# Optimization experiments

Measured on AMD Instinct MI355X. Metric: run time of the kernel, lower is better.

The kernel has to match this reference:

```python
import jax, jax.numpy as jnp
import numpy as np

SCORE = 89; PERF = 300; R = SCORE + PERF   # roll_dims = score_1hot + perf_1hot
H = 1024; Z = 256; B = 64; T = 256
DUR, DY, IOI = 0, 100, 200                 # perf segment boundaries (durratio/dy/ioi)
BN_EPS = 1e-5

PARAM_SHAPES = [
    ("w_ih_f", (3*H, R)), ("w_hh_f", (3*H, H)), ("b_ih_f", (3*H,)), ("b_hh_f", (3*H,)),
    ("w_ih_b", (3*H, R)), ("w_hh_b", (3*H, H)), ("b_ih_b", (3*H,)), ("b_hh_b", (3*H,)),
    ("w_mu", (Z, 2*H)), ("b_mu", (Z,)), ("w_var", (Z, 2*H)), ("b_var", (Z,)),
    ("w_init", (H, Z)), ("b_init", (H,)),
    ("w_ih0", (3*H, Z + R)), ("w_hh0", (3*H, H)), ("b_ih0", (3*H,)), ("b_hh0", (3*H,)),
    ("w_ih1", (3*H, H)), ("w_hh1", (3*H, H)), ("b_ih1", (3*H,)), ("b_hh1", (3*H,)),
    ("w_ih2", (3*H, H)), ("w_hh2", (3*H, H)), ("b_ih2", (3*H,)), ("b_hh2", (3*H,)),
    ("w_out", (PERF, H)), ("b_out", (PERF,)),
]


def gru_cell(x, h, w_ih, w_hh, b_ih, b_hh):
    # torch GRU/GRUCell gate order: r, z, n
    gi = x @ w_ih.T + b_ih
    gh = h @ w_hh.T + b_hh
    i_r, i_z, i_n = jnp.split(gi, 3, axis=-1)
    h_r, h_z, h_n = jnp.split(gh, 3, axis=-1)
    r = jax.nn.sigmoid(i_r + h_r)
    zg = jax.nn.sigmoid(i_z + h_z)
    n = jnp.tanh(i_n + r * h_n)
    return (1.0 - zg) * n + zg * h


def setup_inputs() -> dict:
    key = jax.random.key(0)
    ks = jax.random.split(key, len(PARAM_SHAPES) + 1)
    inp = {"x": jax.random.normal(ks[0], (T, B, R), dtype=jnp.float32),
           "x_lengths": T}
    for i, (nm, shp) in enumerate(PARAM_SHAPES):
        inp[nm] = jax.random.normal(ks[i + 1], shp, dtype=jnp.float32) * 0.05
    return inp


def _forward(x, w_ih_f, w_hh_f, b_ih_f, b_hh_f, w_ih_b, w_hh_b, b_ih_b, b_hh_b,
             w_mu, b_mu, w_var, b_var, w_init, b_init,
             w_ih0, w_hh0, b_ih0, b_hh0, w_ih1, w_hh1, b_ih1, b_hh1,
             w_ih2, w_hh2, b_ih2, b_hh2, w_out, b_out):
    # ---- encode: bidirectional GRU, all lengths == T (pack == plain GRU) ----
    h0 = jnp.zeros((B, H), x.dtype)
    def run(xs, w_ih, w_hh, b_ih, b_hh):
        step = lambda h, xt: ((gru_cell(xt, h, w_ih, w_hh, b_ih, b_hh),) * 2)
        hT, _ = jax.lax.scan(step, h0, xs)
        return hT
    h_f = run(x, w_ih_f, w_hh_f, b_ih_f, b_hh_f)
    h_b = run(x[::-1], w_ih_b, w_hh_b, b_ih_b, b_hh_b)
    hidden = jnp.concatenate([h_f, h_b], axis=-1)          # [B, 2H]
    hidden = hidden / jnp.sqrt(1.0 + BN_EPS)               # BatchNorm2d(1) eval, fresh running stats
    mean = hidden @ w_mu.T + b_mu
    stddev = jnp.exp((hidden @ w_var.T + b_var) * 0.5)     # computed as in torch (unused in eval)
    z = mean                                               # eval-mode reparameterize -> mean
    score = x[:, :, :SCORE]                                # [T, B, SCORE]
    out0 = jnp.zeros((B, PERF), x.dtype).at[:, -1].set(1.0)
    sc0 = jnp.zeros((B, SCORE), x.dtype).at[:, -1].set(1.0)
    hinit = jnp.tanh(z @ w_init.T + b_init)                # hx[0] init
    def step(carry, xj):
        out, sc, hx0, hx1, hx2 = carry
        j, score_j = xj
        inp = jnp.concatenate([out, sc, z], axis=1)        # [B, PERF+SCORE+Z]
        hx0 = gru_cell(inp, hx0, w_ih0, w_hh0, b_ih0, b_hh0)
        hx1 = gru_cell(hx0, jnp.where(j == 0, hx0, hx1), w_ih1, w_hh1, b_ih1, b_hh1)
        hx2 = gru_cell(hx1, jnp.where(j == 0, hx1, hx2), w_ih2, w_hh2, b_ih2, b_hh2)
        logits = hx2 @ w_out.T + b_out                     # [B, PERF]
        o = jnp.concatenate([jax.nn.log_softmax(logits[:, DUR:DY], axis=1),
                             jax.nn.log_softmax(logits[:, DY:IOI], axis=1),
                             jax.nn.log_softmax(logits[:, IOI:], axis=1)], axis=1)
        out_next = jax.nn.one_hot(jnp.argmax(o, axis=1), PERF, dtype=o.dtype)  # eval sampling
        return (out_next, score_j, hx0, hx1, hx2), o
    _, outs = jax.lax.scan(step, (out0, sc0, hinit, hinit, hinit),
                           (jnp.arange(T), score))
    return outs.transpose(1, 0, 2)                         # [B, T, PERF]


def reference(x, x_lengths, w_ih_f, w_hh_f, b_ih_f, b_hh_f, w_ih_b, w_hh_b, b_ih_b, b_hh_b,
              w_mu, b_mu, w_var, b_var, w_init, b_init,
              w_ih0, w_hh0, b_ih0, b_hh0, w_ih1, w_hh1, b_ih1, b_hh1,
              w_ih2, w_hh2, b_ih2, b_hh2, w_out, b_out):
    outs = _forward(x, w_ih_f, w_hh_f, b_ih_f, b_hh_f, w_ih_b, w_hh_b, b_ih_b, b_hh_b,
                    w_mu, b_mu, w_var, b_var, w_init, b_init,
                    w_ih0, w_hh0, b_ih0, b_hh0, w_ih1, w_hh1, b_ih1, b_hh1,
                    w_ih2, w_hh2, b_ih2, b_hh2, w_out, b_out)
    zeros = jnp.zeros((B, Z), x.dtype)  # dis_mean / dis_stddev stay zero in eval branch
    return outs, zeros, zeros
```

## Files before the change

kernel.cpp:

```cpp
#include <hip/hip_runtime.h>
#include <math.h>

namespace {

typedef unsigned long long u64;

constexpr int cH  = 1024;
constexpr int cZ  = 256;
constexpr int cB  = 64;
constexpr int cT  = 256;
constexpr int cR  = 389;
constexpr int cSC = 89;
constexpr int cPF = 300;
constexpr int WSTR = 400;
constexpr float INV_S = 0.9999950000374997f;

__device__ __forceinline__ void fma4(float4& a, const float4 x, const float4 w){
  a.x = fmaf(x.x, w.x, a.x);
  a.y = fmaf(x.y, w.y, a.y);
  a.z = fmaf(x.z, w.z, a.z);
  a.w = fmaf(x.w, w.w, a.w);
}
__device__ __forceinline__ float fold4(const float4 a){ return (a.x + a.y) + (a.z + a.w); }
__device__ __forceinline__ float4 z4(){ return make_float4(0.f, 0.f, 0.f, 0.f); }
__device__ __forceinline__ float sigm(float x){ return 1.f / (1.f + expf(-x)); }

__device__ __forceinline__ void cfence(){ asm volatile("" ::: "memory"); }
__device__ __forceinline__ u64 ld_u64(const u64* p){
  return __hip_atomic_load(p, __ATOMIC_RELAXED, __HIP_MEMORY_SCOPE_AGENT);
}
__device__ __forceinline__ float ld_scal(const float* p){
  return __hip_atomic_load(p, __ATOMIC_RELAXED, __HIP_MEMORY_SCOPE_AGENT);
}
__device__ __forceinline__ void st_scal(float* p, float v){
  __hip_atomic_store(p, v, __ATOMIC_RELAXED, __HIP_MEMORY_SCOPE_AGENT);
}

__device__ __forceinline__ void gbarN(unsigned* base, int sub, unsigned subCnt,
                                      int nsub, unsigned rootCnt){
  __syncthreads();
  if (threadIdx.x == 0){
    cfence();
    unsigned* root = base + nsub * 16;
    unsigned* gen  = base + nsub * 16 + 16;
    const unsigned g = __hip_atomic_load(gen, __ATOMIC_RELAXED, __HIP_MEMORY_SCOPE_AGENT);
    const unsigned a = __hip_atomic_fetch_add(base + sub * 16, 1u,
                         __ATOMIC_RELEASE, __HIP_MEMORY_SCOPE_AGENT);
    bool flip = false;
    if (a == subCnt - 1u){
      const unsigned r = __hip_atomic_fetch_add(root, 1u,
                           __ATOMIC_RELEASE, __HIP_MEMORY_SCOPE_AGENT);
      if (r == rootCnt - 1u){
        for (int t = 0; t < nsub; ++t)
          __hip_atomic_store(base + t * 16, 0u, __ATOMIC_RELAXED, __HIP_MEMORY_SCOPE_AGENT);
        __hip_atomic_store(root, 0u, __ATOMIC_RELAXED, __HIP_MEMORY_SCOPE_AGENT);
        __hip_atomic_store(gen, g + 1u, __ATOMIC_RELEASE, __HIP_MEMORY_SCOPE_AGENT);
        flip = true;
      }
    }
    if (!flip){
      while (__hip_atomic_load(gen, __ATOMIC_RELAXED, __HIP_MEMORY_SCOPE_AGENT) == g)
        __builtin_amdgcn_s_sleep(1);
    }
    cfence();
  }
  __syncthreads();
}

__global__ __launch_bounds__(256) void init_kernel(float* hf0, float* hb0, float* dout_tail,
                                                   unsigned* barE, unsigned* barD){
  const int idx = blockIdx.x * 256 + threadIdx.x;
  const int stride = gridDim.x * 256;
  for (int i = idx; i < cB * cH; i += stride){ hf0[i] = 0.f; hb0[i] = 0.f; }
  for (int i = idx; i < 2 * cB * cZ; i += stride) dout_tail[i] = 0.f;
  for (int i = idx; i < 2048; i += stride) barE[i] = 0u;
  for (int i = idx; i < 512;  i += stride) barD[i] = 0u;
}

__global__ __launch_bounds__(256) void pad_wih_kernel(const float* __restrict__ w,
                                                      float* __restrict__ wp){
  const int idx = blockIdx.x * 256 + threadIdx.x;
  const int stride = gridDim.x * 256;
  const int n = 3 * cH * WSTR;
  for (int i = idx; i < n; i += stride){
    const int r = i / WSTR, c = i - r * WSTR;
    wp[i] = (c < cR) ? w[(size_t)r * cR + c] : 0.f;
  }
}

__global__ __launch_bounds__(256) void pad_wsc_kernel(const float* __restrict__ w_ih0,
                                                      float* __restrict__ wsc){
  const int idx = blockIdx.x * 256 + threadIdx.x;
  const int stride = gridDim.x * 256;
  const int n = 3 * cH * 96;
  for (int i = idx; i < n; i += stride){
    const int r = i / 96, c = i - r * 96;
    wsc[i] = (c < cSC) ? w_ih0[(size_t)r * 645 + 300 + c] : 0.f;
  }
}

__global__ __launch_bounds__(512, 2) void enc_persist(
    const float* __restrict__ x,
    const float* __restrict__ wihPf, const float* __restrict__ whh_f,
    const float* __restrict__ bih_f, const float* __restrict__ bhh_f,
    const float* __restrict__ wihPb, const float* __restrict__ whh_b,
    const float* __restrict__ bih_b, const float* __restrict__ bhh_b,
    float* __restrict__ hfA, float* __restrict__ hfB,
    float* __restrict__ hbA, float* __restrict__ hbB,
    unsigned* __restrict__ barE)
{
  const int bid   = blockIdx.x;
  const int xcd   = bid & 7;
  const int slot  = bid >> 3;
  const int dir   = slot >> 4;
  const int sub16 = slot & 15;
  const int kblk  = xcd * 8 + (sub16 >> 1);
  const int bhalf = sub16 & 1;
  unsigned* bar   = barE + (dir * 2 + bhalf) * 512;

  const float* wih = dir ? wihPb : wihPf;
  const float* whh = dir ? whh_b : whh_f;
  const float* bih = dir ? bih_b : bih_f;
  const float* bhh = dir ? bhh_b : bhh_f;
  float* bufA = dir ? hbA : hfA;
  float* bufB = dir ? hbB : hfB;

  const int tid   = threadIdx.x;
  const int seg8  = tid >> 6;
  const int dseg  = seg8 & 3;
  const int khalf = seg8 >> 2;
  const int lane  = tid & 63;
  const int tx    = lane & 7;
  const int ty    = lane >> 3;
  const int k0    = kblk * 16;
  const int bbase = bhalf * 32;
  const int kloc  = khalf * 8 + ty;
  const int k     = k0 + kloc;

  __shared__ float part[4][4][16][33];
  __shared__ alignas(16) float sh[32 * 516];

  const float4* w0i = (const float4*)wih + (size_t)k * 100;
  const float4* w1i = (const float4*)wih + (size_t)(cH + k) * 100;
  const float4* w2i = (const float4*)wih + (size_t)(2*cH + k) * 100;
  const float4* w0h = (const float4*)whh + (size_t)k * 256;
  const float4* w1h = (const float4*)whh + (size_t)(cH + k) * 256;
  const float4* w2h = (const float4*)whh + (size_t)(2*cH + k) * 256;
  float4* sh4 = (float4*)sh;

  auto stageE = [&](const float* hin, int p){
    const u64* s8 = (const u64*)hin;
    u64* d8 = (u64*)sh;
    u64 tmp[16];
    #pragma unroll
    for (int i = 0; i < 16; ++i){
      const int e = i * 512 + tid;
      tmp[i] = ld_u64(s8 + (size_t)(bbase + (e >> 8)) * 512 + p * 256 + (e & 255));
    }
    #pragma unroll
    for (int i = 0; i < 16; ++i){
      const int e = i * 512 + tid;
      d8[(e >> 8) * 258 + (e & 255)] = tmp[i];
    }
  };

  for (int t = 0; t < cT; ++t){
    const float* hin = (t & 1) ? bufB : bufA;
    float*      hout = (t & 1) ? bufA : bufB;
    const int tt = dir ? (cT - 1 - t) : t;

    float4 R[4], Z[4], NI[4], NH[4];
    #pragma unroll
    for (int jj = 0; jj < 4; ++jj){ R[jj]=z4(); Z[jj]=z4(); NI[jj]=z4(); NH[jj]=z4(); }

    {
      const float* xb[4];
      #pragma unroll
      for (int jj = 0; jj < 4; ++jj)
        xb[jj] = x + ((size_t)tt * cB + bbase + tx + 8*jj) * cR;
      const int c0 = dseg * 25;
      const int cEnd = c0 + 25;
      const int cSafe = (cEnd < 97) ? cEnd : 97;
      for (int c = c0; c < cSafe; ++c){
        const float4 w0v = w0i[c], w1v = w1i[c], w2v = w2i[c];
        const int d = 4 * c;
        #pragma unroll
        for (int jj = 0; jj < 4; ++jj){
          const float* xr = xb[jj];
          const float4 a = make_float4(xr[d], xr[d+1], xr[d+2], xr[d+3]);
          fma4(R[jj], a, w0v); fma4(Z[jj], a, w1v); fma4(NI[jj], a, w2v);
        }
      }
      for (int c = cSafe; c < cEnd; ++c){
        const float4 w0v = w0i[c], w1v = w1i[c], w2v = w2i[c];
        const int d = 4 * c;
        #pragma unroll
        for (int jj = 0; jj < 4; ++jj){
          const float* xr = xb[jj];
          const float4 a = make_float4(
              (d   < cR) ? xr[d]   : 0.f, (d+1 < cR) ? xr[d+1] : 0.f,
              (d+2 < cR) ? xr[d+2] : 0.f, (d+3 < cR) ? xr[d+3] : 0.f);
          fma4(R[jj], a, w0v); fma4(Z[jj], a, w1v); fma4(NI[jj], a, w2v);
        }
      }
    }

    #pragma unroll 1
    for (int p = 0; p < 2; ++p){
      stageE(hin, p);
      __syncthreads();
      {
        const float4* wp0 = w0h + p * 128;
        const float4* wp1 = w1h + p * 128;
        const float4* wp2 = w2h + p * 128;
        #pragma unroll 4
        for (int c = 0; c < 32; ++c){
          const int cc = dseg * 32 + c;
          const float4 w0v = wp0[cc], w1v = wp1[cc], w2v = wp2[cc];
          #pragma unroll
          for (int jj = 0; jj < 4; ++jj){
            const float4 a = sh4[(tx + 8*jj)*129 + cc];
            fma4(R[jj], a, w0v); fma4(Z[jj], a, w1v); fma4(NH[jj], a, w2v);
          }
        }
      }
      __syncthreads();
    }

    #pragma unroll
    for (int jj = 0; jj < 4; ++jj){
      const int b = tx + 8*jj;
      part[dseg][0][kloc][b] = fold4(R[jj]);
      part[dseg][1][kloc][b] = fold4(Z[jj]);
      part[dseg][2][kloc][b] = fold4(NI[jj]);
      part[dseg][3][kloc][b] = fold4(NH[jj]);
    }
    __syncthreads();
    {
      const int row = tid >> 5, bb = tid & 31;
      float rs=0.f, zs=0.f, nis=0.f, nhs=0.f;
      #pragma unroll
      for (int s = 0; s < 4; ++s){
        rs += part[s][0][row][bb]; zs += part[s][1][row][bb];
        nis += part[s][2][row][bb]; nhs += part[s][3][row][bb];
      }
      const int kk = k0 + row, gb = bbase + bb;
      const float r  = sigm(rs + bih[kk] + bhh[kk]);
      const float zg = sigm(zs + bih[cH + kk] + bhh[cH + kk]);
      const float nn = tanhf(nis + bih[2*cH + kk] + r * (nhs + bhh[2*cH + kk]));
      const float hp = ld_scal(&hin[(size_t)gb * cH + kk]);
      st_scal(&hout[(size_t)gb * cH + kk], (1.f - zg) * nn + zg * hp);
    }
    gbarN(bar, kblk >> 3, 8u, 8, 8u);
  }
}

__global__ __launch_bounds__(512, 2) void dec_persist(
    const float* __restrict__ x,
    const float* __restrict__ hfA, const float* __restrict__ hbA,
    const float* __restrict__ w_mu, const float* __restrict__ b_mu,
    const float* __restrict__ w_init, const float* __restrict__ b_init,
    const float* __restrict__ w_ih0,
    const float* __restrict__ wsc,   const float* __restrict__ w_hh0,
    const float* __restrict__ b_ih0, const float* __restrict__ b_hh0,
    const float* __restrict__ w_ih1, const float* __restrict__ w_hh1,
    const float* __restrict__ b_ih1, const float* __restrict__ b_hh1,
    const float* __restrict__ w_ih2, const float* __restrict__ w_hh2,
    const float* __restrict__ b_ih2, const float* __restrict__ b_hh2,
    const float* __restrict__ w_out, const float* __restrict__ b_out,
    float* __restrict__ h0A, float* __restrict__ h0B,
    float* __restrict__ h1A, float* __restrict__ h1B,
    float* __restrict__ h2A, float* __restrict__ h2B,
    float* __restrict__ gi0z, float* __restrict__ zbuf,
    float* __restrict__ amg,  float* __restrict__ scg,
    float* __restrict__ dout,
    unsigned* __restrict__ barD)
{
  const int bid  = blockIdx.x;
  const int xcd  = bid & 7;
  const int slot = bid >> 3;
  const int kq   = xcd * 16 + (slot >> 1);
  const int bh   = slot & 1;
  const int kbase = kq * 8;
  const int bbase = bh * 32;
  const int tid = threadIdx.x;

  const int seg  = tid >> 6;
  const int lane = tid & 63;
  const int tx   = lane & 7;
  const int ty   = lane >> 3;
  const int k    = kbase + ty;

  __shared__ float part[8][4][8][33];
  __shared__ alignas(16) float stg[16 * 1028];
  __shared__ alignas(16) float scs[32 * 100];
  __shared__ float ams[32];
  __shared__ alignas(16) float hb2[cH];
  __shared__ float lg[cPF];
  __shared__ float gmax[3], glse[3], wbest[8];
  __shared__ int   wbidx[8];

  float4* stg4 = (float4*)stg;

  #define GBD gbarN(barD, bid >> 4, 16u, 16, 16u)

  auto stageH = [&](const float* src, int gb0){
    const u64* s8 = (const u64*)src;
    u64* d8 = (u64*)stg;
    u64 tmp[16];
    #pragma unroll
    for (int i = 0; i < 16; ++i){
      const int e = i * 512 + tid;
      tmp[i] = ld_u64(s8 + (size_t)(gb0 + (e >> 9)) * 512 + (e & 511));
    }
    #pragma unroll
    for (int i = 0; i < 16; ++i){
      const int e = i * 512 + tid;
      d8[(e >> 9) * 514 + (e & 511)] = tmp[i];
    }
  };

  auto accH = [&](const float4* w0, const float4* w1, const float4* w2,
                  float4& A0, float4& A1, float4& B0, float4& B1,
                  float4& C0, float4& C1){
    #pragma unroll 4
    for (int c = 0; c < 32; ++c){
      const int cc = seg * 32 + c;
      const float4 w0v = w0[cc], w1v = w1[cc], w2v = w2[cc];
      const float4 aA = stg4[tx * 257 + cc];
      const float4 aB = stg4[(tx + 8) * 257 + cc];
      fma4(A0, aA, w0v); fma4(B0, aA, w1v); fma4(C0, aA, w2v);
      fma4(A1, aB, w0v); fma4(B1, aB, w1v); fma4(C1, aB, w2v);
    }
  };

  auto reduce_store = [&](const float* bi, const float* bhv,
                          const float* hprev, float* hout){
    __syncthreads();
    if (tid < 256){
      const int row = tid >> 5, b = tid & 31;
      float rs=0.f, zs=0.f, nis=0.f, nhs=0.f;
      #pragma unroll
      for (int s = 0; s < 8; ++s){
        rs += part[s][0][row][b]; zs += part[s][1][row][b];
        nis += part[s][2][row][b]; nhs += part[s][3][row][b];
      }
      const int kk = kbase + row, gb = bbase + b;
      const float r  = sigm(rs + bi[kk] + bhv[kk]);
      const float zg = sigm(zs + bi[cH + kk] + bhv[cH + kk]);
      const float nn = tanhf(nis + bi[2*cH + kk] + r * (nhs + bhv[2*cH + kk]));
      const float hp = ld_scal(&hprev[(size_t)gb * cH + kk]);
      st_scal(&hout[(size_t)gb * cH + kk], (1.f - zg) * nn + zg * hp);
    }
  };

  if (bid < cB){
    const int b = bid;
    float4* hl4 = (float4*)stg;
    hl4[tid] = (tid < 256) ? ((const float4*)hfA)[(size_t)b * 256 + tid]
                           : ((const float4*)hbA)[(size_t)b * 256 + (tid - 256)];
    __syncthreads();
    if (tid < 256){
      const float4* wr = (const float4*)w_mu + (size_t)tid * 512;
      float4 s = z4();
      #pragma unroll 4
      for (int c = 0; c < 512; ++c) fma4(s, hl4[c], wr[c]);
      st_scal(&zbuf[(size_t)b * cZ + tid], b_mu[tid] + fold4(s) * INV_S);
    }
    if (tid == 0) st_scal(&amg[b], 299.f);
    if (tid < 96) st_scal(&scg[(size_t)b * 96 + tid], (tid == 88) ? 1.f : 0.f);
  }
  GBD;
  {
    float* zl = stg;
    {
      u64 tmp[8];
      const u64* zb8 = (const u64*)zbuf;
      u64* zl8 = (u64*)stg;
      #pragma unroll
      for (int q = 0; q < 8; ++q){
        const int e = q * 512 + tid;
        tmp[q] = ld_u64(zb8 + (size_t)(bbase + (e >> 7)) * 128 + (e & 127));
      }
      #pragma unroll
      for (int q = 0; q < 8; ++q){
        const int e = q * 512 + tid;
        zl8[(e >> 7) * 130 + (e & 127)] = tmp[q];
      }
    }
    __syncthreads();
    for (int e = tid; e < 768; e += 512){
      const int g = e >> 8, kr = (e >> 5) & 7, b = e & 31;
      const float* zr = zl + b * 260;
      const float* wrow = w_ih0 + (size_t)(g * cH + kbase + kr) * 645 + 389;
      float s = 0.f;
      #pragma unroll 4
      for (int d = 0; d < cZ; ++d) s = fmaf(zr[d], wrow[d], s);
      st_scal(&gi0z[(size_t)(g * cH + kbase + kr) * 64 + bbase + b], s);
    }
    if (tid < 256){
      const int kr = tid >> 5, b = tid & 31;
      const float4* zr4 = (const float4*)(zl + b * 260);
      const float4* wr4 = (const float4*)w_init + (size_t)(kbase + kr) * 64;
      float4 s = z4();
      #pragma unroll 4
      for (int d = 0; d < 64; ++d) fma4(s, zr4[d], wr4[d]);
      st_scal(&h0A[(size_t)(bbase + b) * cH + kbase + kr],
              tanhf(b_init[kbase + kr] + fold4(s)));
    }
  }
  GBD;

  for (int j = 0; j < cT; ++j){
    const int par = j & 1;
    const float* h0p = par ? h0B : h0A;  float* h0n = par ? h0A : h0B;
    const float* h1p = par ? h1B : h1A;  float* h1n = par ? h1A : h1B;
    const float* h2p = par ? h2B : h2A;  float* h2n = par ? h2A : h2B;

    {
      {
        u64 tmp[3];
        const u64* sg8 = (const u64*)scg;
        u64* sc8 = (u64*)scs;
        #pragma unroll
        for (int i = 0; i < 3; ++i){
          const int e = i * 512 + tid;
          const int row = e / 48, col = e - row * 48;
          tmp[i] = ld_u64(sg8 + (size_t)(bbase + row) * 48 + col);
        }
        #pragma unroll
        for (int i = 0; i < 3; ++i){
          const int e = i * 512 + tid;
          const int row = e / 48, col = e - row * 48;
          sc8[row * 50 + col] = tmp[i];
        }
        if (tid < 32) ams[tid] = ld_scal(&amg[bbase + tid]);
      }
      __syncthreads();

      float4 R[4], Z[4], NI[4], NH[4];
      float sR[4], sZ[4], sNI[4];
      #pragma unroll
      for (int jj = 0; jj < 4; ++jj){
        R[jj]=z4(); Z[jj]=z4(); NI[jj]=z4(); NH[jj]=z4();
        sR[jj]=0.f; sZ[jj]=0.f; sNI[jj]=0.f;
      }
      {
        const float4* ws0 = (const float4*)wsc + (size_t)k * 24;
        const float4* ws1 = (const float4*)wsc + (size_t)(cH + k) * 24;
        const float4* ws2 = (const float4*)wsc + (size_t)(2*cH + k) * 24;
        const float4* sc4 = (const float4*)scs;
        #pragma unroll
        for (int c = 0; c < 3; ++c){
          const int cc = seg * 3 + c;
          const float4 w0v = ws0[cc], w1v = ws1[cc], w2v = ws2[cc];
          #pragma unroll
          for (int jj = 0; jj < 4; ++jj){
            const float4 a = sc4[(tx + 8*jj) * 25 + cc];
            fma4(R[jj], a, w0v); fma4(Z[jj], a, w1v); fma4(NI[jj], a, w2v);
          }
        }
      }
      if (seg == 0){
        #pragma unroll
        for (int jj = 0; jj < 4; ++jj){
          const int b = tx + 8*jj, gb = bbase + b;
          const int am = (int)ams[b];
          sR[jj]  = w_ih0[(size_t)k * 645 + am]
                  + ld_scal(&gi0z[(size_t)k * 64 + gb]);
          sZ[jj]  = w_ih0[(size_t)(cH + k) * 645 + am]
                  + ld_scal(&gi0z[(size_t)(cH + k) * 64 + gb]);
          sNI[jj] = w_ih0[(size_t)(2*cH + k) * 645 + am]
                  + ld_scal(&gi0z[(size_t)(2*cH + k) * 64 + gb]);
        }
      }
      const float4* wh0 = (const float4*)w_hh0 + (size_t)k * 256;
      const float4* wh1 = (const float4*)w_hh0 + (size_t)(cH + k) * 256;
      const float4* wh2 = (const float4*)w_hh0 + (size_t)(2*cH + k) * 256;
      __syncthreads();
      stageH(h0p, bbase);      __syncthreads();
      accH(wh0, wh1, wh2, R[0], R[1], Z[0], Z[1], NH[0], NH[1]);
      __syncthreads();
      stageH(h0p, bbase + 16); __syncthreads();
      accH(wh0, wh1, wh2, R[2], R[3], Z[2], Z[3], NH[2], NH[3]);
      #pragma unroll
      for (int jj = 0; jj < 4; ++jj){
        const int b = tx + 8*jj;
        part[seg][0][ty][b] = fold4(R[jj]) + sR[jj];
        part[seg][1][ty][b] = fold4(Z[jj]) + sZ[jj];
        part[seg][2][ty][b] = fold4(NI[jj]) + sNI[jj];
        part[seg][3][ty][b] = fold4(NH[jj]);
      }
      reduce_store(b_ih0, b_hh0, h0p, h0n);
    }
    GBD;

    #pragma unroll 1
    for (int L = 0; L < 2; ++L){
      const float* inG = (L == 0) ? h0n : h1n;
      const float* pvG = (L == 0) ? (j == 0 ? h0n : h1p) : (j == 0 ? h1n : h2p);
      const float* wih = (L == 0) ? w_ih1 : w_ih2;
      const float* whh = (L == 0) ? w_hh1 : w_hh2;
      const float* bi  = (L == 0) ? b_ih1 : b_ih2;
      const float* bhv = (L == 0) ? b_hh1 : b_hh2;
      float* outG      = (L == 0) ? h1n : h2n;

      float4 R[4], Z[4], NI[4], NH[4];
      #pragma unroll
      for (int jj = 0; jj < 4; ++jj){ R[jj]=z4(); Z[jj]=z4(); NI[jj]=z4(); NH[jj]=z4(); }
      const float4* wi0 = (const float4*)wih + (size_t)k * 256;
      const float4* wi1 = (const float4*)wih + (size_t)(cH + k) * 256;
      const float4* wi2 = (const float4*)wih + (size_t)(2*cH + k) * 256;
      const float4* wh0 = (const float4*)whh + (size_t)k * 256;
      const float4* wh1 = (const float4*)whh + (size_t)(cH + k) * 256;
      const float4* wh2 = (const float4*)whh + (size_t)(2*cH + k) * 256;

      stageH(inG, bbase);      __syncthreads();
      accH(wi0, wi1, wi2, R[0], R[1], Z[0], Z[1], NI[0], NI[1]);
      __syncthreads();
      stageH(inG, bbase + 16); __syncthreads();
      accH(wi0, wi1, wi2, R[2], R[3], Z[2], Z[3], NI[2], NI[3]);
      __syncthreads();
      stageH(pvG, bbase);      __syncthreads();
      accH(wh0, wh1, wh2, R[0], R[1], Z[0], Z[1], NH[0], NH[1]);
      __syncthreads();
      stageH(pvG, bbase + 16); __syncthreads();
      accH(wh0, wh1, wh2, R[2], R[3], Z[2], Z[3], NH[2], NH[3]);
      #pragma unroll
      for (int jj = 0; jj < 4; ++jj){
        const int b = tx + 8*jj;
        part[seg][0][ty][b] = fold4(R[jj]);
        part[seg][1][ty][b] = fold4(Z[jj]);
        part[seg][2][ty][b] = fold4(NI[jj]);
        part[seg][3][ty][b] = fold4(NH[jj]);
      }
      reduce_store(bi, bhv, pvG, outG);
      GBD;
    }

    if (bid < cB){
      const int b = bid;
      ((u64*)hb2)[tid] = ld_u64((const u64*)h2n + (size_t)b * 512 + tid);
      __syncthreads();
      for (int p = tid; p < cPF; p += 512){
        const float4* wr = (const float4*)w_out + (size_t)p * 256;
        const float4* hv = (const float4*)hb2;
        float4 s = z4();
        #pragma unroll 4
        for (int c = 0; c < 256; ++c) fma4(s, hv[c], wr[c]);
        lg[p] = b_out[p] + fold4(s);
      }
      __syncthreads();
      const int w = tid >> 6, l = tid & 63;
      if (w < 3){
        float m = -INFINITY;
        for (int p = w*100 + l; p < w*100 + 100; p += 64) m = fmaxf(m, lg[p]);
        #pragma unroll
        for (int off = 32; off > 0; off >>= 1) m = fmaxf(m, __shfl_xor(m, off));
        float s = 0.f;
        for (int p = w*100 + l; p < w*100 + 100; p += 64) s += expf(lg[p] - m);
        #pragma unroll
        for (int off = 32; off > 0; off >>= 1) s += __shfl_xor(s, off);
        if (l == 0){ gmax[w] = m; glse[w] = logf(s); }
      }
      __syncthreads();
      float best = -INFINITY; int bidx = 0x7fffffff;
      for (int p = tid; p < cPF; p += 512){
        const int g3 = (p >= 200) ? 2 : ((p >= 100) ? 1 : 0);
        const float o = lg[p] - gmax[g3] - glse[g3];
        dout[((size_t)b * cT + j) * cPF + p] = o;
        if (o > best || (o == best && p < bidx)){ best = o; bidx = p; }
      }
      #pragma unroll
      for (int off = 32; off > 0; off >>= 1){
        const float ob = __shfl_xor(best, off);
        const int   oi = __shfl_xor(bidx, off);
        if (ob > best || (ob == best && oi < bidx)){ best = ob; bidx = oi; }
      }
      if (l == 0){ wbest[w] = best; wbidx[w] = bidx; }
      __syncthreads();
      if (tid == 0){
        float bb = wbest[0]; int bi = wbidx[0];
        #pragma unroll
        for (int q = 1; q < 8; ++q)
          if (wbest[q] > bb || (wbest[q] == bb && wbidx[q] < bi)){ bb = wbest[q]; bi = wbidx[q]; }
        st_scal(&amg[b], (float)bi);
      }
      if (tid < 96)
        st_scal(&scg[(size_t)b * 96 + tid],
                (tid < cSC) ? x[((size_t)j * cB + b) * cR + tid] : 0.f);
    }
    GBD;
  }
  #undef GBD
}

}

extern "C" void kernel_launch(void* const* d_in, const int* in_sizes, int n_in,
                              void* d_out, int out_size, void* d_ws, size_t ws_size,
                              hipStream_t stream)
{
  const float* x     = (const float*)d_in[0];
  const float* wih_f = (const float*)d_in[2];
  const float* whh_f = (const float*)d_in[3];
  const float* bih_f = (const float*)d_in[4];
  const float* bhh_f = (const float*)d_in[5];
  const float* wih_b = (const float*)d_in[6];
  const float* whh_b = (const float*)d_in[7];
  const float* bih_b = (const float*)d_in[8];
  const float* bhh_b = (const float*)d_in[9];
  const float* w_mu  = (const float*)d_in[10];
  const float* b_mu  = (const float*)d_in[11];
  const float* w_init= (const float*)d_in[14];
  const float* b_init= (const float*)d_in[15];
  const float* w_ih0 = (const float*)d_in[16];
  const float* w_hh0 = (const float*)d_in[17];
  const float* b_ih0 = (const float*)d_in[18];
  const float* b_hh0 = (const float*)d_in[19];
  const float* w_ih1 = (const float*)d_in[20];
  const float* w_hh1 = (const float*)d_in[21];
  const float* b_ih1 = (const float*)d_in[22];
  const float* b_hh1 = (const float*)d_in[23];
  const float* w_ih2 = (const float*)d_in[24];
  const float* w_hh2 = (const float*)d_in[25];
  const float* b_ih2 = (const float*)d_in[26];
  const float* b_hh2 = (const float*)d_in[27];
  const float* w_out = (const float*)d_in[28];
  const float* b_out = (const float*)d_in[29];
  float* dout = (float*)d_out;

  float* ws = (float*)d_ws;
  float* wihfP = ws; ws += (size_t)3 * cH * WSTR;
  float* wihbP = ws; ws += (size_t)3 * cH * WSTR;
  float* wsc   = ws; ws += (size_t)3 * cH * 96;
  float* gi0z  = ws; ws += (size_t)3 * cH * 64;
  float* hfA = ws; ws += cB * cH;  float* hfB = ws; ws += cB * cH;
  float* hbA = ws; ws += cB * cH;  float* hbB = ws; ws += cB * cH;
  float* h0A = ws; ws += cB * cH;  float* h0B = ws; ws += cB * cH;
  float* h1A = ws; ws += cB * cH;  float* h1B = ws; ws += cB * cH;
  float* h2A = ws; ws += cB * cH;  float* h2B = ws; ws += cB * cH;
  float* zbuf = ws; ws += cB * cZ;
  float* scg  = ws; ws += cB * 96;
  float* amg  = ws; ws += cB;
  ws = (float*)(((uintptr_t)ws + 255) & ~(uintptr_t)255);
  unsigned* barE = (unsigned*)ws;  ws += 2048;
  unsigned* barD = (unsigned*)ws;  ws += 512;

  init_kernel<<<256, 256, 0, stream>>>(hfA, hbA, dout + (size_t)cB * cT * cPF, barE, barD);
  pad_wih_kernel<<<512, 256, 0, stream>>>(wih_f, wihfP);
  pad_wih_kernel<<<512, 256, 0, stream>>>(wih_b, wihbP);
  pad_wsc_kernel<<<512, 256, 0, stream>>>(w_ih0, wsc);

  enc_persist<<<256, 512, 0, stream>>>(
      x,
      wihfP, whh_f, bih_f, bhh_f,
      wihbP, whh_b, bih_b, bhh_b,
      hfA, hfB, hbA, hbB, barE);

  dec_persist<<<256, 512, 0, stream>>>(
      x, hfA, hbA,
      w_mu, b_mu, w_init, b_init,
      w_ih0, wsc, w_hh0, b_ih0, b_hh0,
      w_ih1, w_hh1, b_ih1, b_hh1,
      w_ih2, w_hh2, b_ih2, b_hh2,
      w_out, b_out,
      h0A, h0B, h1A, h1B, h2A, h2B,
      gi0z, zbuf, amg, scg, dout, barD);
}
```

Measured before the change: 51.21 ms.

## Double persistent grid to 512 blocks and distribute output projection across all blocks

Both persistent kernels now launch 512 blocks (launch bounds of 4 blocks per CU), halving the per-block hidden-unit or batch slice. The encoder uses 8-row k blocks, and the decoder uses 16-batch quarters. The x input is pre-padded to 400 columns so encoder loads become float4 without bounds checks. The decoder's output projection, previously done by 64 blocks, is now spread over all blocks, with log-softmax and argmax folded into the next step. The gi0z global buffer is replaced by shared memory. This trades more parallel weight streaming against larger grid barriers (32 blocks per group) and extra padded-x traffic, and relies on 512 blocks being co-resident for the spin barriers.

```diff
diff --git a/kernel.cpp b/kernel.cpp
--- a/kernel.cpp
+++ b/kernel.cpp
@@ -74,7 +74,7 @@
   for (int i = idx; i < cB * cH; i += stride){ hf0[i] = 0.f; hb0[i] = 0.f; }
   for (int i = idx; i < 2 * cB * cZ; i += stride) dout_tail[i] = 0.f;
   for (int i = idx; i < 2048; i += stride) barE[i] = 0u;
-  for (int i = idx; i < 512;  i += stride) barD[i] = 0u;
+  for (int i = idx; i < 1024; i += stride) barD[i] = 0u;
 }
 
 __global__ __launch_bounds__(256) void pad_wih_kernel(const float* __restrict__ w,
@@ -88,6 +88,17 @@
   }
 }
 
+__global__ __launch_bounds__(256) void pad_x_kernel(const float* __restrict__ x,
+                                                    float* __restrict__ xp){
+  const int idx = blockIdx.x * 256 + threadIdx.x;
+  const int stride = gridDim.x * 256;
+  const int n = cT * cB * WSTR;
+  for (int i = idx; i < n; i += stride){
+    const int r = i / WSTR, c = i - r * WSTR;
+    xp[i] = (c < cR) ? x[(size_t)r * cR + c] : 0.f;
+  }
+}
+
 __global__ __launch_bounds__(256) void pad_wsc_kernel(const float* __restrict__ w_ih0,
                                                       float* __restrict__ wsc){
   const int idx = blockIdx.x * 256 + threadIdx.x;
@@ -99,8 +110,8 @@
   }
 }
 
-__global__ __launch_bounds__(512, 2) void enc_persist(
-    const float* __restrict__ x,
+__global__ __launch_bounds__(512, 4) void enc_persist(
+    const float* __restrict__ xp,
     const float* __restrict__ wihPf, const float* __restrict__ whh_f,
     const float* __restrict__ bih_f, const float* __restrict__ bhh_f,
     const float* __restrict__ wihPb, const float* __restrict__ whh_b,
@@ -112,10 +123,10 @@
   const int bid   = blockIdx.x;
   const int xcd   = bid & 7;
   const int slot  = bid >> 3;
-  const int dir   = slot >> 4;
-  const int sub16 = slot & 15;
-  const int kblk  = xcd * 8 + (sub16 >> 1);
-  const int bhalf = sub16 & 1;
+  const int dir   = slot >> 5;
+  const int bhalf = (slot >> 4) & 1;
+  const int k16   = slot & 15;
+  const int kblk  = xcd * 16 + k16;
   unsigned* bar   = barE + (dir * 2 + bhalf) * 512;
 
   const float* wih = dir ? wihPb : wihPf;
@@ -126,19 +137,18 @@
   float* bufB = dir ? hbB : hfB;
 
   const int tid   = threadIdx.x;
-  const int seg8  = tid >> 6;
-  const int dseg  = seg8 & 3;
-  const int khalf = seg8 >> 2;
+  const int seg   = tid >> 6;
   const int lane  = tid & 63;
   const int tx    = lane & 7;
   const int ty    = lane >> 3;
-  const int k0    = kblk * 16;
+  const int kbase = kblk * 8;
   const int bbase = bhalf * 32;
-  const int kloc  = khalf * 8 + ty;
-  const int k     = k0 + kloc;
-
-  __shared__ float part[4][4][16][33];
+  const int k     = kbase + ty;
+
   __shared__ alignas(16) float sh[32 * 516];
+  float4* sh4 = (float4*)sh;
+  float*  part = sh;
+  #define EPART(s,g,r,b) part[(((s)*4+(g))*8+(r))*33+(b)]
 
   const float4* w0i = (const float4*)wih + (size_t)k * 100;
   const float4* w1i = (const float4*)wih + (size_t)(cH + k) * 100;
@@ -146,7 +156,6 @@
   const float4* w0h = (const float4*)whh + (size_t)k * 256;
   const float4* w1h = (const float4*)whh + (size_t)(cH + k) * 256;
   const float4* w2h = (const float4*)whh + (size_t)(2*cH + k) * 256;
-  float4* sh4 = (float4*)sh;
 
   auto stageE = [&](const float* hin, int p){
     const u64* s8 = (const u64*)hin;
@@ -174,32 +183,17 @@
     for (int jj = 0; jj < 4; ++jj){ R[jj]=z4(); Z[jj]=z4(); NI[jj]=z4(); NH[jj]=z4(); }
 
     {
-      const float* xb[4];
+      const float4* xr[4];
       #pragma unroll
       for (int jj = 0; jj < 4; ++jj)
-        xb[jj] = x + ((size_t)tt * cB + bbase + tx + 8*jj) * cR;
-      const int c0 = dseg * 25;
-      const int cEnd = c0 + 25;
-      const int cSafe = (cEnd < 97) ? cEnd : 97;
-      for (int c = c0; c < cSafe; ++c){
+        xr[jj] = (const float4*)xp + (size_t)(tt * cB + bbase + tx + 8*jj) * 100;
+      const int c0 = seg * 13;
+      const int c1 = (c0 + 13 < 100) ? c0 + 13 : 100;
+      for (int c = c0; c < c1; ++c){
         const float4 w0v = w0i[c], w1v = w1i[c], w2v = w2i[c];
-        const int d = 4 * c;
         #pragma unroll
         for (int jj = 0; jj < 4; ++jj){
-          const float* xr = xb[jj];
-          const float4 a = make_float4(xr[d], xr[d+1], xr[d+2], xr[d+3]);
-          fma4(R[jj], a, w0v); fma4(Z[jj], a, w1v); fma4(NI[jj], a, w2v);
-        }
-      }
-      for (int c = cSafe; c < cEnd; ++c){
-        const float4 w0v = w0i[c], w1v = w1i[c], w2v = w2i[c];
-        const int d = 4 * c;
-        #pragma unroll
-        for (int jj = 0; jj < 4; ++jj){
-          const float* xr = xb[jj];
-          const float4 a = make_float4(
-              (d   < cR) ? xr[d]   : 0.f, (d+1 < cR) ? xr[d+1] : 0.f,
-              (d+2 < cR) ? xr[d+2] : 0.f, (d+3 < cR) ? xr[d+3] : 0.f);
+          const float4 a = xr[jj][c];
           fma4(R[jj], a, w0v); fma4(Z[jj], a, w1v); fma4(NI[jj], a, w2v);
         }
       }
@@ -214,8 +208,8 @@
         const float4* wp1 = w1h + p * 128;
         const float4* wp2 = w2h + p * 128;
         #pragma unroll 4
-        for (int c = 0; c < 32; ++c){
-          const int cc = dseg * 32 + c;
+        for (int c = 0; c < 16; ++c){
+          const int cc = seg * 16 + c;
           const float4 w0v = wp0[cc], w1v = wp1[cc], w2v = wp2[cc];
           #pragma unroll
           for (int jj = 0; jj < 4; ++jj){
@@ -230,32 +224,33 @@
     #pragma unroll
     for (int jj = 0; jj < 4; ++jj){
       const int b = tx + 8*jj;
-      part[dseg][0][kloc][b] = fold4(R[jj]);
-      part[dseg][1][kloc][b] = fold4(Z[jj]);
-      part[dseg][2][kloc][b] = fold4(NI[jj]);
-      part[dseg][3][kloc][b] = fold4(NH[jj]);
+      EPART(seg,0,ty,b) = fold4(R[jj]);
+      EPART(seg,1,ty,b) = fold4(Z[jj]);
+      EPART(seg,2,ty,b) = fold4(NI[jj]);
+      EPART(seg,3,ty,b) = fold4(NH[jj]);
     }
     __syncthreads();
-    {
+    if (tid < 256){
       const int row = tid >> 5, bb = tid & 31;
       float rs=0.f, zs=0.f, nis=0.f, nhs=0.f;
       #pragma unroll
-      for (int s = 0; s < 4; ++s){
-        rs += part[s][0][row][bb]; zs += part[s][1][row][bb];
-        nis += part[s][2][row][bb]; nhs += part[s][3][row][bb];
-      }
-      const int kk = k0 + row, gb = bbase + bb;
+      for (int s = 0; s < 8; ++s){
+        rs += EPART(s,0,row,bb); zs += EPART(s,1,row,bb);
+        nis += EPART(s,2,row,bb); nhs += EPART(s,3,row,bb);
+      }
+      const int kk = kbase + row, gb = bbase + bb;
       const float r  = sigm(rs + bih[kk] + bhh[kk]);
       const float zg = sigm(zs + bih[cH + kk] + bhh[cH + kk]);
       const float nn = tanhf(nis + bih[2*cH + kk] + r * (nhs + bhh[2*cH + kk]));
       const float hp = ld_scal(&hin[(size_t)gb * cH + kk]);
       st_scal(&hout[(size_t)gb * cH + kk], (1.f - zg) * nn + zg * hp);
     }
-    gbarN(bar, kblk >> 3, 8u, 8, 8u);
-  }
-}
-
-__global__ __launch_bounds__(512, 2) void dec_persist(
+    gbarN(bar, k16, 8u, 16, 16u);
+  }
+  #undef EPART
+}
+
+__global__ __launch_bounds__(512, 4) void dec_persist(
     const float* __restrict__ x,
     const float* __restrict__ hfA, const float* __restrict__ hbA,
     const float* __restrict__ w_mu, const float* __restrict__ b_mu,
@@ -271,18 +266,17 @@
     float* __restrict__ h0A, float* __restrict__ h0B,
     float* __restrict__ h1A, float* __restrict__ h1B,
     float* __restrict__ h2A, float* __restrict__ h2B,
-    float* __restrict__ gi0z, float* __restrict__ zbuf,
-    float* __restrict__ amg,  float* __restrict__ scg,
+    float* __restrict__ zbuf, float* __restrict__ lgbuf,
     float* __restrict__ dout,
     unsigned* __restrict__ barD)
 {
   const int bid  = blockIdx.x;
   const int xcd  = bid & 7;
   const int slot = bid >> 3;
-  const int kq   = xcd * 16 + (slot >> 1);
-  const int bh   = slot & 1;
+  const int kq   = xcd * 16 + (slot >> 2);
+  const int bq   = slot & 3;
   const int kbase = kq * 8;
-  const int bbase = bh * 32;
+  const int bbase = bq * 16;
   const int tid = threadIdx.x;
 
   const int seg  = tid >> 6;
@@ -291,27 +285,26 @@
   const int ty   = lane >> 3;
   const int k    = kbase + ty;
 
-  __shared__ float part[8][4][8][33];
-  __shared__ alignas(16) float stg[16 * 1028];
-  __shared__ alignas(16) float scs[32 * 100];
-  __shared__ float ams[32];
-  __shared__ alignas(16) float hb2[cH];
-  __shared__ float lg[cPF];
-  __shared__ float gmax[3], glse[3], wbest[8];
-  __shared__ int   wbidx[8];
-
-  float4* stg4 = (float4*)stg;
-
-  #define GBD gbarN(barD, bid >> 4, 16u, 16, 16u)
-
-  auto stageH = [&](const float* src, int gb0){
+  __shared__ alignas(16) float arena[16 * 1028];
+  __shared__ float ams[16];
+  __shared__ float gz[3][8][16];
+
+  float4* stg4 = (float4*)arena;
+  float*  part = arena;
+  #define DPART(s,g,r,b) part[(((s)*4+(g))*8+(r))*17+(b)]
+  float*  scs  = arena + 10240;
+  const float4* sc4 = (const float4*)(arena + 10240);
+
+  #define GBD gbarN(barD, bid >> 4, 16u, 32, 32u)
+
+  auto stageH = [&](const float* src){
     const u64* s8 = (const u64*)src;
-    u64* d8 = (u64*)stg;
+    u64* d8 = (u64*)arena;
     u64 tmp[16];
     #pragma unroll
     for (int i = 0; i < 16; ++i){
       const int e = i * 512 + tid;
-      tmp[i] = ld_u64(s8 + (size_t)(gb0 + (e >> 9)) * 512 + (e & 511));
+      tmp[i] = ld_u64(s8 + (size_t)(bbase + (e >> 9)) * 512 + (e & 511));
     }
     #pragma unroll
     for (int i = 0; i < 16; ++i){
@@ -337,13 +330,13 @@
   auto reduce_store = [&](const float* bi, const float* bhv,
                           const float* hprev, float* hout){
     __syncthreads();
-    if (tid < 256){
-      const int row = tid >> 5, b = tid & 31;
+    if (tid < 128){
+      const int row = tid >> 4, b = tid & 15;
       float rs=0.f, zs=0.f, nis=0.f, nhs=0.f;
       #pragma unroll
       for (int s = 0; s < 8; ++s){
-        rs += part[s][0][row][b]; zs += part[s][1][row][b];
-        nis += part[s][2][row][b]; nhs += part[s][3][row][b];
+        rs += DPART(s,0,row,b); zs += DPART(s,1,row,b);
+        nis += DPART(s,2,row,b); nhs += DPART(s,3,row,b);
       }
       const int kk = kbase + row, gb = bbase + b;
       const float r  = sigm(rs + bi[kk] + bhv[kk]);
@@ -354,9 +347,51 @@
     }
   };
 
+  auto fold16 = [&](int jm1, bool writeAms){
+    const int team = tid >> 5, l32 = tid & 31;
+    const int gb = bbase + team;
+    {
+      const u64* lb8 = (const u64*)lgbuf;
+      u64* lr = (u64*)(arena + team * 312);
+      for (int q = l32; q < 150; q += 32)
+        lr[q] = ld_u64(lb8 + (size_t)gb * 150 + q);
+    }
+    __syncthreads();
+    const float* lgr = arena + team * 312;
+    float m[3], lse[3];
+    #pragma unroll
+    for (int g3 = 0; g3 < 3; ++g3){
+      float mm = -INFINITY;
+      for (int p = g3*100 + l32; p < g3*100 + 100; p += 32) mm = fmaxf(mm, lgr[p]);
+      #pragma unroll
+      for (int off = 16; off > 0; off >>= 1) mm = fmaxf(mm, __shfl_xor(mm, off, 32));
+      float ss = 0.f;
+      for (int p = g3*100 + l32; p < g3*100 + 100; p += 32) ss += expf(lgr[p] - mm);
+      #pragma unroll
+      for (int off = 16; off > 0; off >>= 1) ss += __shfl_xor(ss, off, 32);
+      m[g3] = mm; lse[g3] = logf(ss);
+    }
+    float best = -INFINITY; int bidx = 0x7fffffff;
+    for (int p = l32; p < cPF; p += 32){
+      const int g3 = (p >= 200) ? 2 : ((p >= 100) ? 1 : 0);
+      const float o = lgr[p] - m[g3] - lse[g3];
+      if (kq == 0) dout[((size_t)gb * cT + jm1) * cPF + p] = o;
+      if (o > best || (o == best && p < bidx)){ best = o; bidx = p; }
+    }
+    if (writeAms){
+      #pragma unroll
+      for (int off = 16; off > 0; off >>= 1){
+        const float ob = __shfl_xor(best, off, 32);
+        const int   oi = __shfl_xor(bidx, off, 32);
+        if (ob > best || (ob == best && oi < bidx)){ best = ob; bidx = oi; }
+      }
+      if (l32 == 0) ams[team] = (float)bidx;
+    }
+  };
+
   if (bid < cB){
     const int b = bid;
-    float4* hl4 = (float4*)stg;
+    float4* hl4 = (float4*)arena;
     hl4[tid] = (tid < 256) ? ((const float4*)hfA)[(size_t)b * 256 + tid]
                            : ((const float4*)hbA)[(size_t)b * 256 + (tid - 256)];
     __syncthreads();
@@ -367,40 +402,37 @@
       for (int c = 0; c < 512; ++c) fma4(s, hl4[c], wr[c]);
       st_scal(&zbuf[(size_t)b * cZ + tid], b_mu[tid] + fold4(s) * INV_S);
     }
-    if (tid == 0) st_scal(&amg[b], 299.f);
-    if (tid < 96) st_scal(&scg[(size_t)b * 96 + tid], (tid == 88) ? 1.f : 0.f);
   }
   GBD;
   {
-    float* zl = stg;
     {
-      u64 tmp[8];
+      u64 tmp[4];
       const u64* zb8 = (const u64*)zbuf;
-      u64* zl8 = (u64*)stg;
-      #pragma unroll
-      for (int q = 0; q < 8; ++q){
+      u64* zl8 = (u64*)arena;
+      #pragma unroll
+      for (int q = 0; q < 4; ++q){
         const int e = q * 512 + tid;
         tmp[q] = ld_u64(zb8 + (size_t)(bbase + (e >> 7)) * 128 + (e & 127));
       }
       #pragma unroll
-      for (int q = 0; q < 8; ++q){
+      for (int q = 0; q < 4; ++q){
         const int e = q * 512 + tid;
         zl8[(e >> 7) * 130 + (e & 127)] = tmp[q];
       }
     }
     __syncthreads();
-    for (int e = tid; e < 768; e += 512){
-      const int g = e >> 8, kr = (e >> 5) & 7, b = e & 31;
-      const float* zr = zl + b * 260;
+    if (tid < 384){
+      const int g = tid >> 7, kr = (tid >> 4) & 7, b = tid & 15;
+      const float* zr = arena + b * 260;
       const float* wrow = w_ih0 + (size_t)(g * cH + kbase + kr) * 645 + 389;
       float s = 0.f;
       #pragma unroll 4
       for (int d = 0; d < cZ; ++d) s = fmaf(zr[d], wrow[d], s);
-      st_scal(&gi0z[(size_t)(g * cH + kbase + kr) * 64 + bbase + b], s);
-    }
-    if (tid < 256){
-      const int kr = tid >> 5, b = tid & 31;
-      const float4* zr4 = (const float4*)(zl + b * 260);
+      gz[g][kr][b] = s;
+    }
+    if (tid < 128){
+      const int kr = tid >> 4, b = tid & 15;
+      const float4* zr4 = (const float4*)(arena + b * 260);
       const float4* wr4 = (const float4*)w_init + (size_t)(kbase + kr) * 64;
       float4 s = z4();
       #pragma unroll 4
@@ -408,6 +440,7 @@
       st_scal(&h0A[(size_t)(bbase + b) * cH + kbase + kr],
               tanhf(b_init[kbase + kr] + fold4(s)));
     }
+    __syncthreads();
   }
   GBD;
 
@@ -418,30 +451,24 @@
     const float* h2p = par ? h2B : h2A;  float* h2n = par ? h2A : h2B;
 
     {
-      {
-        u64 tmp[3];
-        const u64* sg8 = (const u64*)scg;
-        u64* sc8 = (u64*)scs;
-        #pragma unroll
-        for (int i = 0; i < 3; ++i){
-          const int e = i * 512 + tid;
-          const int row = e / 48, col = e - row * 48;
-          tmp[i] = ld_u64(sg8 + (size_t)(bbase + row) * 48 + col);
-        }
-        #pragma unroll
-        for (int i = 0; i < 3; ++i){
-          const int e = i * 512 + tid;
-          const int row = e / 48, col = e - row * 48;
-          sc8[row * 50 + col] = tmp[i];
-        }
-        if (tid < 32) ams[tid] = ld_scal(&amg[bbase + tid]);
-      }
-      __syncthreads();
-
-      float4 R[4], Z[4], NI[4], NH[4];
-      float sR[4], sZ[4], sNI[4];
-      #pragma unroll
-      for (int jj = 0; jj < 4; ++jj){
+      if (j == 0){
+        if (tid < 16) ams[tid] = 299.f;
+        const int team = tid >> 5, l32 = tid & 31;
+        for (int c = l32; c < 96; c += 32) scs[team * 100 + c] = (c == 88) ? 1.f : 0.f;
+      } else {
+        fold16(j - 1, true);
+        __syncthreads();
+        const int team = tid >> 5, l32 = tid & 31;
+        const int gb = bbase + team;
+        for (int c = l32; c < 96; c += 32)
+          scs[team * 100 + c] = (c < cSC) ? x[((size_t)(j - 1) * cB + gb) * cR + c] : 0.f;
+      }
+      __syncthreads();
+
+      float4 R[2], Z[2], NI[2], NH[2];
+      float sR[2], sZ[2], sNI[2];
+      #pragma unroll
+      for (int jj = 0; jj < 2; ++jj){
         R[jj]=z4(); Z[jj]=z4(); NI[jj]=z4(); NH[jj]=z4();
         sR[jj]=0.f; sZ[jj]=0.f; sNI[jj]=0.f;
       }
@@ -449,13 +476,12 @@
         const float4* ws0 = (const float4*)wsc + (size_t)k * 24;
         const float4* ws1 = (const float4*)wsc + (size_t)(cH + k) * 24;
         const float4* ws2 = (const float4*)wsc + (size_t)(2*cH + k) * 24;
-        const float4* sc4 = (const float4*)scs;
         #pragma unroll
         for (int c = 0; c < 3; ++c){
           const int cc = seg * 3 + c;
           const float4 w0v = ws0[cc], w1v = ws1[cc], w2v = ws2[cc];
           #pragma unroll
-          for (int jj = 0; jj < 4; ++jj){
+          for (int jj = 0; jj < 2; ++jj){
             const float4 a = sc4[(tx + 8*jj) * 25 + cc];
             fma4(R[jj], a, w0v); fma4(Z[jj], a, w1v); fma4(NI[jj], a, w2v);
           }
@@ -463,33 +489,28 @@
       }
       if (seg == 0){
         #pragma unroll
-        for (int jj = 0; jj < 4; ++jj){
-          const int b = tx + 8*jj, gb = bbase + b;
+        for (int jj = 0; jj < 2; ++jj){
+          const int b = tx + 8*jj;
           const int am = (int)ams[b];
-          sR[jj]  = w_ih0[(size_t)k * 645 + am]
-                  + ld_scal(&gi0z[(size_t)k * 64 + gb]);
-          sZ[jj]  = w_ih0[(size_t)(cH + k) * 645 + am]
-                  + ld_scal(&gi0z[(size_t)(cH + k) * 64 + gb]);
-          sNI[jj] = w_ih0[(size_t)(2*cH + k) * 645 + am]
-                  + ld_scal(&gi0z[(size_t)(2*cH + k) * 64 + gb]);
+          sR[jj]  = w_ih0[(size_t)k * 645 + am]          + gz[0][ty][b];
+          sZ[jj]  = w_ih0[(size_t)(cH + k) * 645 + am]   + gz[1][ty][b];
+          sNI[jj] = w_ih0[(size_t)(2*cH + k) * 645 + am] + gz[2][ty][b];
         }
       }
       const float4* wh0 = (const float4*)w_hh0 + (size_t)k * 256;
       const float4* wh1 = (const float4*)w_hh0 + (size_t)(cH + k) * 256;
       const float4* wh2 = (const float4*)w_hh0 + (size_t)(2*cH + k) * 256;
       __syncthreads();
-      stageH(h0p, bbase);      __syncthreads();
+      stageH(h0p);  __syncthreads();
       accH(wh0, wh1, wh2, R[0], R[1], Z[0], Z[1], NH[0], NH[1]);
       __syncthreads();
-      stageH(h0p, bbase + 16); __syncthreads();
-      accH(wh0, wh1, wh2, R[2], R[3], Z[2], Z[3], NH[2], NH[3]);
-      #pragma unroll
-      for (int jj = 0; jj < 4; ++jj){
+      #pragma unroll
+      for (int jj = 0; jj < 2; ++jj){
         const int b = tx + 8*jj;
-        part[seg][0][ty][b] = fold4(R[jj]) + sR[jj];
-        part[seg][1][ty][b] = fold4(Z[jj]) + sZ[jj];
-        part[seg][2][ty][b] = fold4(NI[jj]) + sNI[jj];
-        part[seg][3][ty][b] = fold4(NH[jj]);
+        DPART(seg,0,ty,b) = fold4(R[jj]) + sR[jj];
+        DPART(seg,1,ty,b) = fold4(Z[jj]) + sZ[jj];
+        DPART(seg,2,ty,b) = fold4(NI[jj]) + sNI[jj];
+        DPART(seg,3,ty,b) = fold4(NH[jj]);
       }
       reduce_store(b_ih0, b_hh0, h0p, h0n);
     }
@@ -505,9 +526,9 @@
       const float* bhv = (L == 0) ? b_hh1 : b_hh2;
       float* outG      = (L == 0) ? h1n : h2n;
 
-      float4 R[4], Z[4], NI[4], NH[4];
-      #pragma unroll
-      for (int jj = 0; jj < 4; ++jj){ R[jj]=z4(); Z[jj]=z4(); NI[jj]=z4(); NH[jj]=z4(); }
+      float4 R[2], Z[2], NI[2], NH[2];
+      #pragma unroll
+      for (int jj = 0; jj < 2; ++jj){ R[jj]=z4(); Z[jj]=z4(); NI[jj]=z4(); NH[jj]=z4(); }
       const float4* wi0 = (const float4*)wih + (size_t)k * 256;
       const float4* wi1 = (const float4*)wih + (size_t)(cH + k) * 256;
       const float4* wi2 = (const float4*)wih + (size_t)(2*cH + k) * 256;
@@ -515,83 +536,52 @@
       const float4* wh1 = (const float4*)whh + (size_t)(cH + k) * 256;
       const float4* wh2 = (const float4*)whh + (size_t)(2*cH + k) * 256;
 
-      stageH(inG, bbase);      __syncthreads();
+      stageH(inG);  __syncthreads();
       accH(wi0, wi1, wi2, R[0], R[1], Z[0], Z[1], NI[0], NI[1]);
       __syncthreads();
-      stageH(inG, bbase + 16); __syncthreads();
-      accH(wi0, wi1, wi2, R[2], R[3], Z[2], Z[3], NI[2], NI[3]);
-      __syncthreads();
-      stageH(pvG, bbase);      __syncthreads();
+      stageH(pvG);  __syncthreads();
       accH(wh0, wh1, wh2, R[0], R[1], Z[0], Z[1], NH[0], NH[1]);
       __syncthreads();
-      stageH(pvG, bbase + 16); __syncthreads();
-      accH(wh0, wh1, wh2, R[2], R[3], Z[2], Z[3], NH[2], NH[3]);
-      #pragma unroll
-      for (int jj = 0; jj < 4; ++jj){
+      #pragma unroll
+      for (int jj = 0; jj < 2; ++jj){
         const int b = tx + 8*jj;
-        part[seg][0][ty][b] = fold4(R[jj]);
-        part[seg][1][ty][b] = fold4(Z[jj]);
-        part[seg][2][ty][b] = fold4(NI[jj]);
-        part[seg][3][ty][b] = fold4(NH[jj]);
+        DPART(seg,0,ty,b) = fold4(R[jj]);
+        DPART(seg,1,ty,b) = fold4(Z[jj]);
+        DPART(seg,2,ty,b) = fold4(NI[jj]);
+        DPART(seg,3,ty,b) = fold4(NH[jj]);
       }
       reduce_store(bi, bhv, pvG, outG);
       GBD;
     }
 
-    if (bid < cB){
-      const int b = bid;
-      ((u64*)hb2)[tid] = ld_u64((const u64*)h2n + (size_t)b * 512 + tid);
-      __syncthreads();
-      for (int p = tid; p < cPF; p += 512){
-        const float4* wr = (const float4*)w_out + (size_t)p * 256;
-        const float4* hv = (const float4*)hb2;
+    {
+      const int p0 = (kq * 300) >> 7;
+      const int p1 = ((kq + 1) * 300) >> 7;
+      stageH(h2n);  __syncthreads();
+      const int b16 = tid >> 5;
+      const int cs  = tid & 31;
+      for (int pr = p0; pr < p1; ++pr){
+        const float4* wr = (const float4*)w_out + (size_t)pr * 256;
+        const float4* av = stg4 + b16 * 257;
         float4 s = z4();
-        #pragma unroll 4
-        for (int c = 0; c < 256; ++c) fma4(s, hv[c], wr[c]);
-        lg[p] = b_out[p] + fold4(s);
-      }
-      __syncthreads();
-      const int w = tid >> 6, l = tid & 63;
-      if (w < 3){
-        float m = -INFINITY;
-        for (int p = w*100 + l; p < w*100 + 100; p += 64) m = fmaxf(m, lg[p]);
         #pragma unroll
-        for (int off = 32; off > 0; off >>= 1) m = fmaxf(m, __shfl_xor(m, off));
-        float s = 0.f;
-        for (int p = w*100 + l; p < w*100 + 100; p += 64) s += expf(lg[p] - m);
+        for (int u = 0; u < 8; ++u){
+          const int cc = cs + u * 32;
+          fma4(s, av[cc], wr[cc]);
+        }
+        float v = fold4(s);
         #pragma unroll
-        for (int off = 32; off > 0; off >>= 1) s += __shfl_xor(s, off);
-        if (l == 0){ gmax[w] = m; glse[w] = logf(s); }
-      }
-      __syncthreads();
-      float best = -INFINITY; int bidx = 0x7fffffff;
-      for (int p = tid; p < cPF; p += 512){
-        const int g3 = (p >= 200) ? 2 : ((p >= 100) ? 1 : 0);
-        const float o = lg[p] - gmax[g3] - glse[g3];
-        dout[((size_t)b * cT + j) * cPF + p] = o;
-        if (o > best || (o == best && p < bidx)){ best = o; bidx = p; }
-      }
-      #pragma unroll
-      for (int off = 32; off > 0; off >>= 1){
-        const float ob = __shfl_xor(best, off);
-        const int   oi = __shfl_xor(bidx, off);
-        if (ob > best || (ob == best && oi < bidx)){ best = ob; bidx = oi; }
-      }
-      if (l == 0){ wbest[w] = best; wbidx[w] = bidx; }
-      __syncthreads();
-      if (tid == 0){
-        float bb = wbest[0]; int bi = wbidx[0];
-        #pragma unroll
-        for (int q = 1; q < 8; ++q)
-          if (wbest[q] > bb || (wbest[q] == bb && wbidx[q] < bi)){ bb = wbest[q]; bi = wbidx[q]; }
-        st_scal(&amg[b], (float)bi);
-      }
-      if (tid < 96)
-        st_scal(&scg[(size_t)b * 96 + tid],
-                (tid < cSC) ? x[((size_t)j * cB + b) * cR + tid] : 0.f);
+        for (int off = 16; off > 0; off >>= 1) v += __shfl_xor(v, off, 32);
+        if (cs == 0)
+          st_scal(&lgbuf[(size_t)(bbase + b16) * cPF + pr], v + b_out[pr]);
+      }
+      __syncthreads();
     }
     GBD;
   }
+
+  if (kq == 0) fold16(cT - 1, false);
+  #undef DPART
   #undef GBD
 }
 
@@ -633,32 +623,32 @@
   float* ws = (float*)d_ws;
   float* wihfP = ws; ws += (size_t)3 * cH * WSTR;
   float* wihbP = ws; ws += (size_t)3 * cH * WSTR;
+  float* xp    = ws; ws += (size_t)cT * cB * WSTR;
   float* wsc   = ws; ws += (size_t)3 * cH * 96;
-  float* gi0z  = ws; ws += (size_t)3 * cH * 64;
   float* hfA = ws; ws += cB * cH;  float* hfB = ws; ws += cB * cH;
   float* hbA = ws; ws += cB * cH;  float* hbB = ws; ws += cB * cH;
   float* h0A = ws; ws += cB * cH;  float* h0B = ws; ws += cB * cH;
   float* h1A = ws; ws += cB * cH;  float* h1B = ws; ws += cB * cH;
   float* h2A = ws; ws += cB * cH;  float* h2B = ws; ws += cB * cH;
-  float* zbuf = ws; ws += cB * cZ;
-  float* scg  = ws; ws += cB * 96;
-  float* amg  = ws; ws += cB;
+  float* zbuf  = ws; ws += cB * cZ;
+  float* lgbuf = ws; ws += cB * cPF;
   ws = (float*)(((uintptr_t)ws + 255) & ~(uintptr_t)255);
   unsigned* barE = (unsigned*)ws;  ws += 2048;
-  unsigned* barD = (unsigned*)ws;  ws += 512;
+  unsigned* barD = (unsigned*)ws;  ws += 1024;
 
   init_kernel<<<256, 256, 0, stream>>>(hfA, hbA, dout + (size_t)cB * cT * cPF, barE, barD);
   pad_wih_kernel<<<512, 256, 0, stream>>>(wih_f, wihfP);
   pad_wih_kernel<<<512, 256, 0, stream>>>(wih_b, wihbP);
+  pad_x_kernel<<<2048, 256, 0, stream>>>(x, xp);
   pad_wsc_kernel<<<512, 256, 0, stream>>>(w_ih0, wsc);
 
-  enc_persist<<<256, 512, 0, stream>>>(
-      x,
+  enc_persist<<<512, 512, 0, stream>>>(
+      xp,
       wihfP, whh_f, bih_f, bhh_f,
       wihbP, whh_b, bih_b, bhh_b,
       hfA, hfB, hbA, hbB, barE);
 
-  dec_persist<<<256, 512, 0, stream>>>(
+  dec_persist<<<512, 512, 0, stream>>>(
       x, hfA, hbA,
       w_mu, b_mu, w_init, b_init,
       w_ih0, wsc, w_hh0, b_ih0, b_hh0,
@@ -666,5 +656,5 @@
       w_ih2, w_hh2, b_ih2, b_hh2,
       w_out, b_out,
       h0A, h0B, h1A, h1B, h2A, h2B,
-      gi0z, zbuf, amg, scg, dout, barD);
-}
+      zbuf, lgbuf, dout, barD);
+}
```

After: 82.53 ms. 1.61x slower.
